# Kernel optimization log

Hardware: AMD Instinct MI355X
Metric: run time of the kernel (lower is better)

## Reference

```python
import jax, jax.numpy as jnp
import numpy as np

# ---- configuration matching init_kwargs ----
D_IN, D_HID, D_OUT = 4096, 4096, 4096
INTRINSIC = 1024            # size of trainable vector V
BATCH = 512
Q = float(min(np.log(60000.0) ** 2 / INTRINSIC, 1.0))  # fastJL_vars: q = min(ln(60000)^2/d, 1)

PARAM_SHAPES = {
    'W1': (D_HID, D_IN),   # nn.Linear weight is (out, in)
    'b1': (D_HID,),
    'W2': (D_OUT, D_HID),
    'b2': (D_OUT,),
}

def _next_pow2(n):
    return 1 << int(np.ceil(np.log2(n)))

def fwht(x):
    """Fast Walsh-Hadamard transform over a length-2^k vector.
    Mirrors fast_walsh_hadamard_torched: at step i, split axis i of the
    [2]*k view into halves a,b and concatenate (a+b, a-b)."""
    n = x.shape[0]
    steps = int(round(np.log2(n)))
    for i in range(steps):
        y = x.reshape(2 ** i, 2, -1)
        a, b = y[:, 0], y[:, 1]
        x = jnp.stack([a + b, a - b], axis=1).reshape(n)
    return x

def fastjl(V, D, PP, shape):
    """ret = (1/dd) * (PP * FWHT(D * pad(V, LL)))[:DD], reshaped to param shape."""
    LL = D.shape[0]
    dd = V.shape[0]
    DD = int(np.prod(shape))
    v_pad = jnp.zeros((LL,), V.dtype).at[:dd].set(V)
    h = fwht(D * v_pad)
    return ((PP * h)[:DD] / dd).reshape(shape)

def setup_inputs() -> dict:
    key = jax.random.key(0)
    ks = jax.random.split(key, 4 + 3 * len(PARAM_SHAPES) + len(PARAM_SHAPES))
    inp = {}
    inp['x'] = jax.random.normal(ks[0], (BATCH, D_IN), dtype=jnp.float32)
    inp['V'] = jax.random.normal(ks[1], (INTRINSIC,), dtype=jnp.float32) * 0.01
    i = 2
    for name, shape in PARAM_SHAPES.items():
        # initial (frozen) parameter values
        scale = 1.0 / np.sqrt(shape[-1]) if len(shape) > 1 else 0.0
        inp[name + '_init'] = jax.random.normal(ks[i], shape, dtype=jnp.float32) * scale
        LL = _next_pow2(int(np.prod(shape)))
        # D: Rademacher +-1
        rad = jax.random.bernoulli(ks[i + 1], 0.5, (LL,))
        inp['D_' + name] = jnp.where(rad, 1.0, -1.0).astype(jnp.float32)
        # PP = B * R, B ~ Bernoulli(1-q), R ~ N(0, (1/q)^2)
        B = jax.random.bernoulli(ks[i + 2], 1.0 - Q, (LL,)).astype(jnp.float32)
        R = jax.random.normal(ks[i + 3], (LL,), dtype=jnp.float32) * (1.0 / Q)
        inp['PP_' + name] = B * R
        i += 4
    return inp

def reference(x, V, W1_init, b1_init, W2_init, b2_init,
              D_W1, PP_W1, D_b1, PP_b1, D_W2, PP_W2, D_b2, PP_b2):
    # Reconstruct each wrapped-module parameter: init + FastJL(V)
    W1 = W1_init + fastjl(V, D_W1, PP_W1, PARAM_SHAPES['W1'])
    b1 = b1_init + fastjl(V, D_b1, PP_b1, PARAM_SHAPES['b1'])
    W2 = W2_init + fastjl(V, D_W2, PP_W2, PARAM_SHAPES['W2'])
    b2 = b2_init + fastjl(V, D_b2, PP_b2, PARAM_SHAPES['b2'])
    # wrapped module forward: Linear -> ReLU -> Linear
    h = jax.nn.relu(x @ W1.T + b1)
    return h @ W2.T + b2
```

## Files before the change

kernel.cpp:

```cpp
#include <hip/hip_runtime.h>
#include <hip/hip_bf16.h>
#include <stdint.h>

typedef unsigned short u16;
typedef __attribute__((ext_vector_type(8))) short short8;
typedef __attribute__((ext_vector_type(4))) float f32x4;

__device__ __forceinline__ uint32_t f2bf(float f) {
    union { float f; uint32_t u; } c; c.f = f;
    uint32_t u = c.u;
    u += 0x7fffu + ((u >> 16) & 1u);
    return u >> 16;
}

__device__ __forceinline__ void glds16(const void* g, void* l) {
    __builtin_amdgcn_global_load_lds(
        (const __attribute__((address_space(1))) uint32_t*)g,
        (__attribute__((address_space(3))) uint32_t*)l,
        16, 0, 0);
}

__global__ void fwht_g_kernel(const float* __restrict__ V,
                              const float* __restrict__ D0, const float* __restrict__ D1,
                              const float* __restrict__ D2, const float* __restrict__ D3,
                              float* __restrict__ g) {
    __shared__ float s[1024];
    int t = threadIdx.x;
    const float* D = (blockIdx.x == 0) ? D0 : (blockIdx.x == 1) ? D1 :
                     (blockIdx.x == 2) ? D2 : D3;
    s[t] = D[t] * V[t];
    __syncthreads();
    #pragma unroll
    for (int st = 512; st >= 1; st >>= 1) {
        float a = s[t];
        float b = s[t ^ st];
        __syncthreads();
        s[t] = (t & st) ? (b - a) : (a + b);
        __syncthreads();
    }
    g[blockIdx.x * 1024 + t] = s[t] * (1.0f / 1024.0f);
}

__global__ void bias_kernel(const float* __restrict__ init, const float* __restrict__ PP,
                            const float* __restrict__ g, float* __restrict__ out, int n) {
    int i = blockIdx.x * blockDim.x + threadIdx.x;
    if (i < n) out[i] = init[i] + PP[i] * g[i & 1023];
}

__global__ void cast_kernel(const float* __restrict__ in, u16* __restrict__ out, int n4) {
    int i = blockIdx.x * blockDim.x + threadIdx.x;
    if (i >= n4) return;
    float4 v = ((const float4*)in)[i];
    uint32_t lo = f2bf(v.x) | (f2bf(v.y) << 16);
    uint32_t hi = f2bf(v.z) | (f2bf(v.w) << 16);
    ((uint2*)out)[i] = make_uint2(lo, hi);
}

__global__ void wmat_kernel(const float* __restrict__ init, const float* __restrict__ PP,
                            const float* __restrict__ g, u16* __restrict__ out, int n4) {
    int i = blockIdx.x * blockDim.x + threadIdx.x;
    if (i >= n4) return;
    int e = i * 4;
    float4 wi = ((const float4*)init)[i];
    float4 pp = ((const float4*)PP)[i];
    float4 gv = *((const float4*)(g + (e & 1023)));
    uint32_t lo = f2bf(wi.x + pp.x * gv.x) | (f2bf(wi.y + pp.y * gv.y) << 16);
    uint32_t hi = f2bf(wi.z + pp.z * gv.z) | (f2bf(wi.w + pp.w * gv.w) << 16);
    ((uint2*)out)[i] = make_uint2(lo, hi);
}

__global__ __launch_bounds__(256, 4) void gemm_splitk(const u16* __restrict__ A,
                                                      const u16* __restrict__ B,
                                                      float* __restrict__ P,
                                                      int M, int N, int K, int Kslice) {
    constexpr int BM = 128, BN = 64, BK = 64;
    __shared__ u16 As[BM * BK];
    __shared__ u16 Bs[BN * BK];

    const int t    = threadIdx.x;
    const int wid  = t >> 6;
    const int lane = t & 63;
    const int wr   = wid >> 1;
    const int wc   = wid & 1;
    const int fr   = lane & 15;
    const int fq   = lane >> 4;
    const int rx   = (fr & 7) << 4;

    const int bn = blockIdx.x, bm = blockIdx.y, sk = blockIdx.z;
    const int k_beg = sk * Kslice;

    const u16* Abase = A + (size_t)(bm * BM) * K;
    const u16* Bbase = B + (size_t)(bn * BN) * K;

    f32x4 acc[4][2];
    #pragma unroll
    for (int m = 0; m < 4; ++m)
        #pragma unroll
        for (int n = 0; n < 2; ++n)
            acc[m][n] = (f32x4){0.f, 0.f, 0.f, 0.f};

    #pragma unroll 1
    for (int k0 = k_beg; k0 < k_beg + Kslice; k0 += BK) {
        #pragma unroll
        for (int q = 0; q < 4; ++q) {
            int L = q * 256 + t;
            int row = L >> 3;
            int cg  = (L & 7) ^ (row & 7);
            glds16(Abase + (size_t)row * K + k0 + cg * 8, As + L * 8);
        }
        #pragma unroll
        for (int q = 0; q < 2; ++q) {
            int L = q * 256 + t;
            int row = L >> 3;
            int cg  = (L & 7) ^ (row & 7);
            glds16(Bbase + (size_t)row * K + k0 + cg * 8, Bs + L * 8);
        }
        __syncthreads();

        const char* Ap = (const char*)As;
        const char* Bp = (const char*)Bs;
        __builtin_amdgcn_s_setprio(1);
        #pragma unroll
        for (int ks = 0; ks < 2; ++ks) {
            const int co = (ks * 64 + fq * 16) ^ rx;
            short8 a[4], b[2];
            #pragma unroll
            for (int m = 0; m < 4; ++m)
                a[m] = *(const short8*)(Ap + (wr * 64 + m * 16 + fr) * 128 + co);
            #pragma unroll
            for (int n = 0; n < 2; ++n)
                b[n] = *(const short8*)(Bp + (wc * 32 + n * 16 + fr) * 128 + co);
            #pragma unroll
            for (int m = 0; m < 4; ++m)
                #pragma unroll
                for (int n = 0; n < 2; ++n)
                    acc[m][n] = __builtin_amdgcn_mfma_f32_16x16x32_bf16(a[m], b[n], acc[m][n], 0, 0, 0);
        }
        __builtin_amdgcn_s_setprio(0);
        __syncthreads();
    }

    float* Pp = P + (size_t)sk * M * N;
    #pragma unroll
    for (int m = 0; m < 4; ++m) {
        int grow0 = bm * BM + wr * 64 + m * 16 + fq * 4;
        #pragma unroll
        for (int n = 0; n < 2; ++n) {
            int gcol = bn * BN + wc * 32 + n * 16 + fr;
            #pragma unroll
            for (int j = 0; j < 4; ++j)
                Pp[(size_t)(grow0 + j) * N + gcol] = acc[m][n][j];
        }
    }
}

template <typename OutT, bool RELU, int S>
__global__ void reduce_kernel(const float* __restrict__ P, const float* __restrict__ bias,
                              OutT* __restrict__ out, int MN, int N) {
    int i = blockIdx.x * blockDim.x + threadIdx.x;
    if (i * 4 >= MN) return;
    int e = i * 4;
    int col = e & (N - 1);
    float4 acc = ((const float4*)(P + e))[0];
    #pragma unroll
    for (int s = 1; s < S; ++s) {
        float4 p = ((const float4*)(P + (size_t)s * MN + e))[0];
        acc.x += p.x; acc.y += p.y; acc.z += p.z; acc.w += p.w;
    }
    float4 bv = *((const float4*)(bias + col));
    acc.x += bv.x; acc.y += bv.y; acc.z += bv.z; acc.w += bv.w;
    if (RELU) {
        acc.x = fmaxf(acc.x, 0.f); acc.y = fmaxf(acc.y, 0.f);
        acc.z = fmaxf(acc.z, 0.f); acc.w = fmaxf(acc.w, 0.f);
    }
    if constexpr (sizeof(OutT) == 2) {
        uint32_t lo = f2bf(acc.x) | (f2bf(acc.y) << 16);
        uint32_t hi = f2bf(acc.z) | (f2bf(acc.w) << 16);
        ((uint2*)out)[i] = make_uint2(lo, hi);
    } else {
        ((float4*)out)[i] = acc;
    }
}

extern "C" void kernel_launch(void* const* d_in, const int* in_sizes, int n_in,
                              void* d_out, int out_size, void* d_ws, size_t ws_size,
                              hipStream_t stream) {
    (void)in_sizes; (void)n_in; (void)out_size; (void)ws_size;

    const float* x       = (const float*)d_in[0];
    const float* V       = (const float*)d_in[1];
    const float* W1_init = (const float*)d_in[2];
    const float* D_W1    = (const float*)d_in[3];
    const float* PP_W1   = (const float*)d_in[4];
    const float* b1_init = (const float*)d_in[5];
    const float* D_b1    = (const float*)d_in[6];
    const float* PP_b1   = (const float*)d_in[7];
    const float* W2_init = (const float*)d_in[8];
    const float* D_W2    = (const float*)d_in[9];
    const float* PP_W2   = (const float*)d_in[10];
    const float* b2_init = (const float*)d_in[11];
    const float* D_b2    = (const float*)d_in[12];
    const float* PP_b2   = (const float*)d_in[13];

    constexpr size_t MB = 1024 * 1024;
    char* ws = (char*)d_ws;
    float* g    = (float*)(ws);
    float* b1w  = (float*)(ws + 16384);
    float* b2w  = (float*)(ws + 32768);
    u16*   xb   = (u16*)(ws + 65536);
    u16*   hb   = (u16*)(ws + 65536 + 4 * MB);
    u16*   wbuf = (u16*)(ws + 65536 + 8 * MB);
    float* Pbuf = (float*)(ws + 65536 + 40 * MB);

    const int M = 512, N = 4096, K = 4096, S = 4, Kslice = K / S;

    fwht_g_kernel<<<4, 1024, 0, stream>>>(V, D_W1, D_b1, D_W2, D_b2, g);
    bias_kernel<<<4, 1024, 0, stream>>>(b1_init, PP_b1, g + 1024, b1w, 4096);
    bias_kernel<<<4, 1024, 0, stream>>>(b2_init, PP_b2, g + 3072, b2w, 4096);
    cast_kernel<<<2048, 256, 0, stream>>>(x, xb, M * K / 4);

    wmat_kernel<<<16384, 256, 0, stream>>>(W1_init, PP_W1, g, wbuf, 4096 * 4096 / 4);
    gemm_splitk<<<dim3(N / 64, M / 128, S), 256, 0, stream>>>(xb, wbuf, Pbuf, M, N, K, Kslice);
    reduce_kernel<u16, true, S><<<M * N / 4 / 256, 256, 0, stream>>>(Pbuf, b1w, hb, M * N, N);

    wmat_kernel<<<16384, 256, 0, stream>>>(W2_init, PP_W2, g + 2048, wbuf, 4096 * 4096 / 4);
    gemm_splitk<<<dim3(N / 64, M / 128, S), 256, 0, stream>>>(hb, wbuf, Pbuf, M, N, K, Kslice);
    reduce_kernel<float, false, S><<<M * N / 4 / 256, 256, 0, stream>>>(Pbuf, b2w, (float*)d_out, M * N, N);
}
```

Baseline: 133.9 us.

## Overlap W2 materialization with first GEMM in a combined interleaved kernel

```diff
diff --git a/kernel.cpp b/kernel.cpp
--- a/kernel.cpp
+++ b/kernel.cpp
@@ -69,87 +69,115 @@
     ((uint2*)out)[i] = make_uint2(lo, hi);
 }
 
+#define GEMM_BODY(As, Bs, A_, B_, P_, bn_, bm_, sk_, K_, Kslice_)                  \
+    do {                                                                            \
+        const int t    = threadIdx.x;                                               \
+        const int wid  = t >> 6;                                                    \
+        const int lane = t & 63;                                                    \
+        const int wr   = wid >> 1;                                                  \
+        const int wc   = wid & 1;                                                   \
+        const int fr   = lane & 15;                                                 \
+        const int fq   = lane >> 4;                                                 \
+        const int rx   = (fr & 7) << 4;                                             \
+        const int k_beg = (sk_) * (Kslice_);                                        \
+        const u16* Abase = (A_) + (size_t)((bm_) * 128) * (K_);                     \
+        const u16* Bbase = (B_) + (size_t)((bn_) * 64) * (K_);                      \
+        f32x4 acc[4][2];                                                            \
+        _Pragma("unroll")                                                           \
+        for (int m = 0; m < 4; ++m)                                                 \
+            _Pragma("unroll")                                                       \
+            for (int n = 0; n < 2; ++n)                                             \
+                acc[m][n] = (f32x4){0.f, 0.f, 0.f, 0.f};                            \
+        _Pragma("unroll 1")                                                         \
+        for (int k0 = k_beg; k0 < k_beg + (Kslice_); k0 += 64) {                    \
+            _Pragma("unroll")                                                       \
+            for (int q = 0; q < 4; ++q) {                                           \
+                int L = q * 256 + t;                                                \
+                int row = L >> 3;                                                   \
+                int cg  = (L & 7) ^ (row & 7);                                      \
+                glds16(Abase + (size_t)row * (K_) + k0 + cg * 8, As + L * 8);       \
+            }                                                                       \
+            _Pragma("unroll")                                                       \
+            for (int q = 0; q < 2; ++q) {                                           \
+                int L = q * 256 + t;                                                \
+                int row = L >> 3;                                                   \
+                int cg  = (L & 7) ^ (row & 7);                                      \
+                glds16(Bbase + (size_t)row * (K_) + k0 + cg * 8, Bs + L * 8);       \
+            }                                                                       \
+            __syncthreads();                                                        \
+            const char* Ap = (const char*)As;                                       \
+            const char* Bp = (const char*)Bs;                                       \
+            __builtin_amdgcn_s_setprio(1);                                          \
+            _Pragma("unroll")                                                       \
+            for (int ks = 0; ks < 2; ++ks) {                                        \
+                const int co = (ks * 64 + fq * 16) ^ rx;                            \
+                short8 a[4], b[2];                                                  \
+                _Pragma("unroll")                                                   \
+                for (int m = 0; m < 4; ++m)                                         \
+                    a[m] = *(const short8*)(Ap + (wr * 64 + m * 16 + fr) * 128 + co); \
+                _Pragma("unroll")                                                   \
+                for (int n = 0; n < 2; ++n)                                         \
+                    b[n] = *(const short8*)(Bp + (wc * 32 + n * 16 + fr) * 128 + co); \
+                _Pragma("unroll")                                                   \
+                for (int m = 0; m < 4; ++m)                                         \
+                    _Pragma("unroll")                                               \
+                    for (int n = 0; n < 2; ++n)                                     \
+                        acc[m][n] = __builtin_amdgcn_mfma_f32_16x16x32_bf16(        \
+                            a[m], b[n], acc[m][n], 0, 0, 0);                        \
+            }                                                                       \
+            __builtin_amdgcn_s_setprio(0);                                          \
+            __syncthreads();                                                        \
+        }                                                                           \
+        float* Pp = (P_) + (size_t)(sk_) * 512 * 4096;                              \
+        _Pragma("unroll")                                                           \
+        for (int m = 0; m < 4; ++m) {                                               \
+            int grow0 = (bm_) * 128 + wr * 64 + m * 16 + fq * 4;                    \
+            _Pragma("unroll")                                                       \
+            for (int n = 0; n < 2; ++n) {                                           \
+                int gcol = (bn_) * 64 + wc * 32 + n * 16 + fr;                      \
+                _Pragma("unroll")                                                   \
+                for (int j = 0; j < 4; ++j)                                         \
+                    Pp[(size_t)(grow0 + j) * 4096 + gcol] = acc[m][n][j];           \
+            }                                                                       \
+        }                                                                           \
+    } while (0)
+
 __global__ __launch_bounds__(256, 4) void gemm_splitk(const u16* __restrict__ A,
                                                       const u16* __restrict__ B,
                                                       float* __restrict__ P,
-                                                      int M, int N, int K, int Kslice) {
-    constexpr int BM = 128, BN = 64, BK = 64;
-    __shared__ u16 As[BM * BK];
-    __shared__ u16 Bs[BN * BK];
-
-    const int t    = threadIdx.x;
-    const int wid  = t >> 6;
-    const int lane = t & 63;
-    const int wr   = wid >> 1;
-    const int wc   = wid & 1;
-    const int fr   = lane & 15;
-    const int fq   = lane >> 4;
-    const int rx   = (fr & 7) << 4;
-
+                                                      int K, int Kslice) {
+    __shared__ u16 As[128 * 64];
+    __shared__ u16 Bs[64 * 64];
     const int bn = blockIdx.x, bm = blockIdx.y, sk = blockIdx.z;
-    const int k_beg = sk * Kslice;
-
-    const u16* Abase = A + (size_t)(bm * BM) * K;
-    const u16* Bbase = B + (size_t)(bn * BN) * K;
-
-    f32x4 acc[4][2];
-    #pragma unroll
-    for (int m = 0; m < 4; ++m)
-        #pragma unroll
-        for (int n = 0; n < 2; ++n)
-            acc[m][n] = (f32x4){0.f, 0.f, 0.f, 0.f};
-
-    #pragma unroll 1
-    for (int k0 = k_beg; k0 < k_beg + Kslice; k0 += BK) {
-        #pragma unroll
-        for (int q = 0; q < 4; ++q) {
-            int L = q * 256 + t;
-            int row = L >> 3;
-            int cg  = (L & 7) ^ (row & 7);
-            glds16(Abase + (size_t)row * K + k0 + cg * 8, As + L * 8);
-        }
-        #pragma unroll
-        for (int q = 0; q < 2; ++q) {
-            int L = q * 256 + t;
-            int row = L >> 3;
-            int cg  = (L & 7) ^ (row & 7);
-            glds16(Bbase + (size_t)row * K + k0 + cg * 8, Bs + L * 8);
-        }
-        __syncthreads();
-
-        const char* Ap = (const char*)As;
-        const char* Bp = (const char*)Bs;
-        __builtin_amdgcn_s_setprio(1);
-        #pragma unroll
-        for (int ks = 0; ks < 2; ++ks) {
-            const int co = (ks * 64 + fq * 16) ^ rx;
-            short8 a[4], b[2];
-            #pragma unroll
-            for (int m = 0; m < 4; ++m)
-                a[m] = *(const short8*)(Ap + (wr * 64 + m * 16 + fr) * 128 + co);
-            #pragma unroll
-            for (int n = 0; n < 2; ++n)
-                b[n] = *(const short8*)(Bp + (wc * 32 + n * 16 + fr) * 128 + co);
-            #pragma unroll
-            for (int m = 0; m < 4; ++m)
-                #pragma unroll
-                for (int n = 0; n < 2; ++n)
-                    acc[m][n] = __builtin_amdgcn_mfma_f32_16x16x32_bf16(a[m], b[n], acc[m][n], 0, 0, 0);
-        }
-        __builtin_amdgcn_s_setprio(0);
-        __syncthreads();
-    }
-
-    float* Pp = P + (size_t)sk * M * N;
-    #pragma unroll
-    for (int m = 0; m < 4; ++m) {
-        int grow0 = bm * BM + wr * 64 + m * 16 + fq * 4;
-        #pragma unroll
-        for (int n = 0; n < 2; ++n) {
-            int gcol = bn * BN + wc * 32 + n * 16 + fr;
-            #pragma unroll
-            for (int j = 0; j < 4; ++j)
-                Pp[(size_t)(grow0 + j) * N + gcol] = acc[m][n][j];
+    GEMM_BODY(As, Bs, A, B, P, bn, bm, sk, K, Kslice);
+}
+
+__global__ __launch_bounds__(256, 4) void gemm1_wmat2(const u16* __restrict__ A,
+                                                      const u16* __restrict__ B,
+                                                      float* __restrict__ P,
+                                                      const float* __restrict__ W2init,
+                                                      const float* __restrict__ PP2,
+                                                      const float* __restrict__ g2,
+                                                      u16* __restrict__ w2out,
+                                                      int K, int Kslice, int nwmat) {
+    __shared__ u16 As[128 * 64];
+    __shared__ u16 Bs[64 * 64];
+    const int bid = blockIdx.x;
+    const int id  = bid >> 1;
+    if ((bid & 1) == 0) {
+        const int bn = id & 63, bm = (id >> 6) & 3, sk = id >> 8;
+        GEMM_BODY(As, Bs, A, B, P, bn, bm, sk, K, Kslice);
+    } else {
+        const int t = threadIdx.x;
+        const int stride = nwmat * 256;
+        for (int i = id * 256 + t; i < 4096 * 4096 / 4; i += stride) {
+            int e = i * 4;
+            float4 wi = ((const float4*)W2init)[i];
+            float4 pp = ((const float4*)PP2)[i];
+            float4 gv = *((const float4*)(g2 + (e & 1023)));
+            uint32_t lo = f2bf(wi.x + pp.x * gv.x) | (f2bf(wi.y + pp.y * gv.y) << 16);
+            uint32_t hi = f2bf(wi.z + pp.z * gv.z) | (f2bf(wi.w + pp.w * gv.w) << 16);
+            ((uint2*)w2out)[i] = make_uint2(lo, hi);
         }
     }
 }
@@ -185,7 +213,7 @@
 extern "C" void kernel_launch(void* const* d_in, const int* in_sizes, int n_in,
                               void* d_out, int out_size, void* d_ws, size_t ws_size,
                               hipStream_t stream) {
-    (void)in_sizes; (void)n_in; (void)out_size; (void)ws_size;
+    (void)in_sizes; (void)n_in; (void)out_size;
 
     const float* x       = (const float*)d_in[0];
     const float* V       = (const float*)d_in[1];
@@ -204,15 +232,17 @@
 
     constexpr size_t MB = 1024 * 1024;
     char* ws = (char*)d_ws;
-    float* g    = (float*)(ws);
-    float* b1w  = (float*)(ws + 16384);
-    float* b2w  = (float*)(ws + 32768);
-    u16*   xb   = (u16*)(ws + 65536);
-    u16*   hb   = (u16*)(ws + 65536 + 4 * MB);
-    u16*   wbuf = (u16*)(ws + 65536 + 8 * MB);
-    float* Pbuf = (float*)(ws + 65536 + 40 * MB);
+    float* g     = (float*)(ws);
+    float* b1w   = (float*)(ws + 16384);
+    float* b2w   = (float*)(ws + 32768);
+    u16*   xb    = (u16*)(ws + 65536);
+    u16*   hb    = (u16*)(ws + 65536 + 4 * MB);
+    u16*   wbuf  = (u16*)(ws + 65536 + 8 * MB);
+    float* Pbuf  = (float*)(ws + 65536 + 40 * MB);
+    u16*   w2buf = (u16*)(ws + 65536 + 72 * MB);
 
     const int M = 512, N = 4096, K = 4096, S = 4, Kslice = K / S;
+    const bool overlap = ws_size >= (size_t)(65536 + 104 * MB);
 
     fwht_g_kernel<<<4, 1024, 0, stream>>>(V, D_W1, D_b1, D_W2, D_b2, g);
     bias_kernel<<<4, 1024, 0, stream>>>(b1_init, PP_b1, g + 1024, b1w, 4096);
@@ -220,10 +250,19 @@
     cast_kernel<<<2048, 256, 0, stream>>>(x, xb, M * K / 4);
 
     wmat_kernel<<<16384, 256, 0, stream>>>(W1_init, PP_W1, g, wbuf, 4096 * 4096 / 4);
-    gemm_splitk<<<dim3(N / 64, M / 128, S), 256, 0, stream>>>(xb, wbuf, Pbuf, M, N, K, Kslice);
-    reduce_kernel<u16, true, S><<<M * N / 4 / 256, 256, 0, stream>>>(Pbuf, b1w, hb, M * N, N);
-
-    wmat_kernel<<<16384, 256, 0, stream>>>(W2_init, PP_W2, g + 2048, wbuf, 4096 * 4096 / 4);
-    gemm_splitk<<<dim3(N / 64, M / 128, S), 256, 0, stream>>>(hb, wbuf, Pbuf, M, N, K, Kslice);
-    reduce_kernel<float, false, S><<<M * N / 4 / 256, 256, 0, stream>>>(Pbuf, b2w, (float*)d_out, M * N, N);
-}
+
+    if (overlap) {
+        gemm1_wmat2<<<2048, 256, 0, stream>>>(xb, wbuf, Pbuf,
+                                              W2_init, PP_W2, g + 2048, w2buf,
+                                              K, Kslice, 1024);
+        reduce_kernel<u16, true, S><<<M * N / 4 / 256, 256, 0, stream>>>(Pbuf, b1w, hb, M * N, N);
+        gemm_splitk<<<dim3(N / 64, M / 128, S), 256, 0, stream>>>(hb, w2buf, Pbuf, K, Kslice);
+        reduce_kernel<float, false, S><<<M * N / 4 / 256, 256, 0, stream>>>(Pbuf, b2w, (float*)d_out, M * N, N);
+    } else {
+        gemm_splitk<<<dim3(N / 64, M / 128, S), 256, 0, stream>>>(xb, wbuf, Pbuf, K, Kslice);
+        reduce_kernel<u16, true, S><<<M * N / 4 / 256, 256, 0, stream>>>(Pbuf, b1w, hb, M * N, N);
+        wmat_kernel<<<16384, 256, 0, stream>>>(W2_init, PP_W2, g + 2048, wbuf, 4096 * 4096 / 4);
+        gemm_splitk<<<dim3(N / 64, M / 128, S), 256, 0, stream>>>(hb, wbuf, Pbuf, K, Kslice);
+        reduce_kernel<float, false, S><<<M * N / 4 / 256, 256, 0, stream>>>(Pbuf, b2w, (float*)d_out, M * N, N);
+    }
+}
```

After: 139.1 us. 1.04x slower.
